# Optimization experiments

Hardware: AMD Instinct MI355X
Metric: run time of the kernel (lower is better)

Reference implementation:

```python
import jax, jax.numpy as jnp
import numpy as np


def _ln(x, g, b, eps=1e-5):
    mu = jnp.mean(x, axis=-1, keepdims=True)
    var = jnp.mean((x - mu) ** 2, axis=-1, keepdims=True)
    return (x - mu) * jax.lax.rsqrt(var + eps) * g + b


def setup_inputs() -> dict:
    key = jax.random.key(0)
    ks = jax.random.split(key, 12)
    B, H, W, D = 16, 128, 128, 64
    N = H * W
    Dff = 4 * D
    s = 0.02
    f32 = jnp.float32
    return {
        "x": jax.random.normal(ks[0], (B, N, D), f32),
        "H": H,
        "W": W,
        "ln1_scale": jnp.ones((D,), f32),
        "ln1_bias": jnp.zeros((D,), f32),
        "Wk": jax.random.normal(ks[1], (D, D), f32) * s,
        "bk": jnp.zeros((D,), f32),
        "Wq": jax.random.normal(ks[2], (D, D), f32) * s,
        "bq": jnp.zeros((D,), f32),
        "Wv": jax.random.normal(ks[3], (D, D), f32) * s,
        "bv": jnp.zeros((D,), f32),
        "Wr": jax.random.normal(ks[4], (D, D), f32) * s,
        "br": jnp.zeros((D,), f32),
        "ln2_scale": jnp.ones((D,), f32),
        "ln2_bias": jnp.zeros((D,), f32),
        "W1": jax.random.normal(ks[5], (Dff, D), f32) * s,
        "b1": jnp.zeros((Dff,), f32),
        "dw_w": jax.random.normal(ks[6], (Dff, 1, 3, 3), f32) * s,
        "dw_b": jnp.zeros((Dff,), f32),
        "W2": jax.random.normal(ks[7], (D, Dff), f32) * s,
        "b2": jnp.zeros((D,), f32),
    }


def reference(x, H, W, ln1_scale, ln1_bias, Wk, bk, Wq, bq, Wv, bv, Wr, br,
              ln2_scale, ln2_bias, W1, b1, dw_w, dw_b, W2, b2):
    B, N, D = x.shape
    Dff = W1.shape[0]

    # ---- EfficientAttention (head_count=1), tokens kept as [B, N, C] ----
    n1 = _ln(x, ln1_scale, ln1_bias)
    # 1x1 convs on [B,D,H,W] == per-token linear projections
    k = jax.nn.softmax(n1 @ Wk.T + bk, axis=1)    # softmax over spatial dim N (torch dim=2 of [B,Ck,N])
    q = jax.nn.softmax(n1 @ Wq.T + bq, axis=-1)   # softmax over key channels (torch dim=1)
    v = n1 @ Wv.T + bv                            # [B,N,Cv]
    context = jnp.einsum('bnk,bnv->bkv', k, v)    # key @ value^T, tiny [B,Ck,Cv]
    att = jnp.einsum('bkv,bnk->bnv', context, q)  # context^T @ query -> [B,N,Cv]
    attn_out = att @ Wr.T + br                    # reprojection 1x1 conv
    tx = x + attn_out

    # ---- MixFFN: fc1 -> depthwise 3x3 -> GELU -> fc2 ----
    n2 = _ln(tx, ln2_scale, ln2_bias)
    h = n2 @ W1.T + b1                            # [B,N,Dff]
    himg = jnp.transpose(h, (0, 2, 1)).reshape(B, Dff, H, W)
    conv = jax.lax.conv_general_dilated(
        himg, dw_w, window_strides=(1, 1), padding='SAME',
        feature_group_count=Dff,
        dimension_numbers=('NCHW', 'OIHW', 'NCHW')) + dw_b[None, :, None, None]
    h2 = jnp.transpose(conv.reshape(B, Dff, N), (0, 2, 1))
    h2 = jax.nn.gelu(h2, approximate=False)       # torch nn.GELU default is exact erf
    out = tx + (h2 @ W2.T + b2)
    return out
```

## Files before the change

### kernel.cpp

```cpp
#include <hip/hip_runtime.h>
#include <math.h>

typedef __bf16 bf16x8 __attribute__((ext_vector_type(8)));
typedef float f32x4 __attribute__((ext_vector_type(4)));
typedef float f32x2 __attribute__((ext_vector_type(2)));
typedef unsigned short u16x8 __attribute__((ext_vector_type(8)));
typedef unsigned short u16x4v __attribute__((ext_vector_type(4)));

constexpr int NIMG = 16384;
constexpr int HPITCH = 130;

__device__ __forceinline__ unsigned short f2bf(float f){
  unsigned u = __builtin_bit_cast(unsigned, f);
  u += 0x7fffu + ((u>>16)&1u);
  return (unsigned short)(u>>16);
}
__device__ __forceinline__ unsigned pack2(float a, float b){
  return (unsigned)f2bf(a) | ((unsigned)f2bf(b)<<16);
}
__device__ __forceinline__ float bf2f(unsigned short h){
  unsigned u = ((unsigned)h)<<16;
  return __builtin_bit_cast(float, u);
}
__device__ __forceinline__ bf16x8 ldfrag_g(const unsigned short* p){
  u16x8 v = *reinterpret_cast<const u16x8*>(p);
  return __builtin_bit_cast(bf16x8, v);
}
__device__ __forceinline__ f32x4 mfma16(bf16x8 a, bf16x8 b, f32x4 c){
  return __builtin_amdgcn_mfma_f32_16x16x32_bf16(a, b, c, 0, 0, 0);
}


__global__ __launch_bounds__(64) void k0_wfrag(
  const float* __restrict__ Wk, const float* __restrict__ Wq,
  const float* __restrict__ Wv, const float* __restrict__ Wr,
  const float* __restrict__ W1, const float* __restrict__ W2,
  const float* __restrict__ dww, const float* __restrict__ dwb,
  float* __restrict__ dwp, unsigned short* __restrict__ wf)
{
  const int bid = blockIdx.x, l = threadIdx.x;
  if (bid == 96){
    #pragma unroll
    for (int c=0;c<4;++c){
      int cp = l*4 + c;
      int f = ((cp&15)<<4) | (cp>>4);
      #pragma unroll
      for (int j=0;j<9;++j) dwp[cp*12 + j] = dww[f*9+j];
      dwp[cp*12 + 9]  = dwb[f];
      dwp[cp*12 + 10] = 0.f;
      dwp[cp*12 + 11] = 0.f;
    }
    return;
  }
  const float* src; int K, nt, ks; unsigned short* dst; bool perm = false;
  if (bid < 32){
    int w = bid>>3, f = bid&7;
    src = (w==0)?Wk:(w==1)?Wq:(w==2)?Wv:Wr;
    K = 64; nt = f>>1; ks = f&1;
    dst = wf + w*4096 + f*512;
  } else if (bid < 64){
    int f = bid-32; src = W1; K = 64; nt = f>>1; ks = f&1;
    dst = wf + 16384 + f*512;
  } else {
    int f = bid-64; src = W2; K = 256; nt = f>>3; ks = f&7;
    dst = wf + 32768 + f*512; perm = true;
  }
  u16x8 v;
  #pragma unroll
  for (int j=0;j<8;++j){
    int k = ks*32 + (l>>4)*8 + j;
    if (perm) k = ((k&15)<<4) | (k>>4);
    int n = nt*16 + (l&15);
    v[j] = f2bf(src[n*K + k]);
  }
  *reinterpret_cast<u16x8*>(dst + l*8) = v;
}

__global__ __launch_bounds__(256) void zhalo(unsigned* __restrict__ gh, unsigned* __restrict__ zr){
  int idx = blockIdx.x*256 + threadIdx.x;
  if (idx < 262144){
    int ch = idx & 63;
    int pos = idx >> 6;
    int side = pos & 1, row = pos >> 1;
    gh[(size_t)(row*HPITCH + side*(HPITCH-1))*64 + ch] = 0;
  } else {
    int j = idx - 262144;
    if (j < 8320) zr[j] = 0;
  }
}

__global__ __launch_bounds__(256,2) void k1_ctx(
  const float* __restrict__ x, const float* __restrict__ g1, const float* __restrict__ be1,
  const float* __restrict__ bk, const float* __restrict__ bv,
  const unsigned short* __restrict__ wf,
  float* __restrict__ g_part, float* __restrict__ g_sump)
{
  __shared__ unsigned short tiles[4][4096];
  __shared__ float ctx_l[64*68];
  __shared__ float ssum_l[4][64];
  const int t = threadIdx.x, wid = t>>6, l = t&63;
  const int lg = l>>4, l15 = l&15;
  unsigned short* tile = tiles[wid];
  const int tok0 = blockIdx.x*512 + wid*128;

  bf16x8 WkF[8], WvF[8];
  #pragma unroll
  for (int f=0; f<8; ++f){
    WkF[f] = ldfrag_g(wf +    0 + f*512 + l*8);
    WvF[f] = ldfrag_g(wf + 8192 + f*512 + l*8);
  }
  float4 g1v  = *reinterpret_cast<const float4*>(&g1[l15*4]);
  float4 be1v = *reinterpret_cast<const float4*>(&be1[l15*4]);
  float bkv[4], bvv[4];
  #pragma unroll
  for (int ct=0; ct<4; ++ct){ bkv[ct]=bk[ct*16+l15]; bvv[ct]=bv[ct*16+l15]; }

  f32x4 acc[4][4];
  #pragma unroll
  for (int a=0;a<4;++a)
    #pragma unroll
    for (int b=0;b<4;++b) acc[a][b] = (f32x4){0.f,0.f,0.f,0.f};
  float sume[4] = {0.f,0.f,0.f,0.f};

  for (int tb=0; tb<2; ++tb){
    const int tbase = tok0 + tb*64;
    #pragma unroll
    for (int it=0; it<16; ++it){
      int row = it*4 + lg;
      float4 xv = *reinterpret_cast<const float4*>(&x[(size_t)(tbase+row)*64 + l15*4]);
      float s1 = xv.x+xv.y+xv.z+xv.w;
      float s2 = xv.x*xv.x + xv.y*xv.y + xv.z*xv.z + xv.w*xv.w;
      #pragma unroll
      for (int off=1; off<16; off<<=1){ s1 += __shfl_xor(s1,off,64); s2 += __shfl_xor(s2,off,64); }
      float mu = s1*(1.f/64.f);
      float rs = rsqrtf(s2*(1.f/64.f) - mu*mu + 1e-5f);
      uint2 pk = { pack2((xv.x-mu)*rs*g1v.x + be1v.x, (xv.y-mu)*rs*g1v.y + be1v.y),
                   pack2((xv.z-mu)*rs*g1v.z + be1v.z, (xv.w-mu)*rs*g1v.w + be1v.w) };
      *reinterpret_cast<uint2*>(&tile[row*64 + ((l15*4) ^ ((row&7)<<3))]) = pk;
    }
    bf16x8 aF[4][2];
    #pragma unroll
    for (int mt=0;mt<4;++mt){
      int row = mt*16+l15, sw=(row&7)<<3, ab=row*64;
      aF[mt][0] = __builtin_bit_cast(bf16x8, *reinterpret_cast<const u16x8*>(tile+ab+((     lg*8)^sw)));
      aF[mt][1] = __builtin_bit_cast(bf16x8, *reinterpret_cast<const u16x8*>(tile+ab+((32 + lg*8)^sw)));
    }
    #pragma unroll
    for (int half=0; half<2; ++half){
      #pragma unroll
      for (int m2=0;m2<2;++m2){
        const int mt = half*2+m2;
        #pragma unroll
        for (int ct=0;ct<4;++ct){
          f32x4 z = {0.f,0.f,0.f,0.f};
          z = mfma16(aF[mt][0], WkF[ct*2+0], z);
          z = mfma16(aF[mt][1], WkF[ct*2+1], z);
          float e0=__expf(z[0]+bkv[ct]), e1=__expf(z[1]+bkv[ct]);
          float e2=__expf(z[2]+bkv[ct]), e3=__expf(z[3]+bkv[ct]);
          sume[ct] += (e0+e1)+(e2+e3);
          const int c = ct*16+l15, sw = (c&7)<<3;
          const int cb = m2*16+lg*4;
          uint2 pe = { pack2(e0,e1), pack2(e2,e3) };
          *reinterpret_cast<uint2*>(&tile[c*64 + (cb ^ sw)]) = pe;
          f32x4 w = {0.f,0.f,0.f,0.f};
          w = mfma16(aF[mt][0], WvF[ct*2+0], w);
          w = mfma16(aF[mt][1], WvF[ct*2+1], w);
          uint2 pv = { pack2(w[0]+bvv[ct], w[1]+bvv[ct]), pack2(w[2]+bvv[ct], w[3]+bvv[ct]) };
          *reinterpret_cast<uint2*>(&tile[c*64 + ((32+cb) ^ sw)]) = pv;
        }
      }
      bf16x8 eA[4], vB[4];
      #pragma unroll
      for (int cm=0;cm<4;++cm){
        int row = cm*16+l15, sw=(row&7)<<3;
        eA[cm] = __builtin_bit_cast(bf16x8, *reinterpret_cast<const u16x8*>(tile + row*64 + ((     lg*8)^sw)));
        vB[cm] = __builtin_bit_cast(bf16x8, *reinterpret_cast<const u16x8*>(tile + row*64 + ((32 + lg*8)^sw)));
      }
      #pragma unroll
      for (int cm=0; cm<4; ++cm)
        #pragma unroll
        for (int jn=0; jn<4; ++jn)
          acc[cm][jn] = mfma16(eA[cm], vB[jn], acc[cm][jn]);
    }
  }
  #pragma unroll
  for (int ct=0; ct<4; ++ct){
    float s = sume[ct];
    s += __shfl_xor(s,16,64); s += __shfl_xor(s,32,64);
    if (lg==0) ssum_l[wid][ct*16+l15] = s;
  }
  #define CTX_RED(OP) \
    _Pragma("unroll") for (int cm=0;cm<4;++cm) \
    _Pragma("unroll") for (int jn=0;jn<4;++jn) \
    _Pragma("unroll") for (int r=0;r<4;++r) \
      ctx_l[(cm*16+lg*4+r)*68 + jn*16+l15] OP acc[cm][jn][r];
  if (wid==0){ CTX_RED(=) }  __syncthreads();
  if (wid==1){ CTX_RED(+=) } __syncthreads();
  if (wid==2){ CTX_RED(+=) } __syncthreads();
  if (wid==3){ CTX_RED(+=) } __syncthreads();
  #undef CTX_RED
  for (int i=t; i<4096; i+=256)
    g_part[(size_t)blockIdx.x*4096 + i] = ctx_l[(i>>6)*68 + (i&63)];
  if (t<64)
    g_sump[blockIdx.x*64 + t] = ssum_l[0][t]+ssum_l[1][t]+ssum_l[2][t]+ssum_l[3][t];
}

__global__ __launch_bounds__(512) void k15_ctxwr(
  const float* __restrict__ g_part, const float* __restrict__ g_sump,
  const float* __restrict__ Wr, unsigned short* __restrict__ ctxWrF)
{
  __shared__ float sctx[4096];
  __shared__ float sWr[4096];
  __shared__ float sinv[64];
  const int b = blockIdx.x, t = threadIdx.x;
  if (t<64){
    float s=0.f;
    #pragma unroll 8
    for (int p=0;p<32;++p) s += g_sump[(b*32+p)*64 + t];
    sinv[t] = 1.f/s;
  }
  for (int idx=t; idx<4096; idx+=512){
    float s=0.f;
    #pragma unroll 8
    for (int p=0;p<32;++p) s += g_part[(size_t)(b*32+p)*4096 + idx];
    sctx[idx] = s;
  }
  __syncthreads();
  {
    int c = t>>3, d0 = (t&7)*8;
    float invc = sinv[c];
    #pragma unroll
    for (int dd=0; dd<8; ++dd){
      int d = d0+dd; float s = 0.f;
      #pragma unroll
      for (int v=0; v<64; ++v) s += sctx[c*64+v]*Wr[d*64+v];
      sWr[c*64+d] = s*invc;
    }
  }
  __syncthreads();
  {
    int f = t>>6, l = t&63, nt = f>>1, ks = f&1;
    u16x8 v;
    #pragma unroll
    for (int j=0;j<8;++j){
      int k = ks*32 + (l>>4)*8 + j;
      int n = nt*16 + (l&15);
      v[j] = f2bf(sWr[k*64+n]);
    }
    *reinterpret_cast<u16x8*>(ctxWrF + b*4096 + f*512 + l*8) = v;
  }
}

__global__ __launch_bounds__(256,2) void k2_attn_ffn1(
  const float* __restrict__ x,
  const float* __restrict__ g1, const float* __restrict__ be1,
  const float* __restrict__ bq, const float* __restrict__ br,
  const float* __restrict__ g2, const float* __restrict__ be2,
  const float* __restrict__ b1,
  const unsigned short* __restrict__ wf,
  const unsigned short* __restrict__ ctxWrF,
  unsigned short* __restrict__ g_txb, unsigned char* __restrict__ g_h)
{
  __shared__ unsigned short tiles[4][4096];
  const int t = threadIdx.x, wid = t>>6, l = t&63;
  const int l15 = l&15, lg = l>>4;
  unsigned short* tile = tiles[wid];
  const int tok0 = (blockIdx.x*4 + wid)*64;
  const int img  = blockIdx.x>>6;
  const int yrow = (tok0>>7)&127;
  const int xb   = tok0&127;
  const size_t hbase = ((size_t)(img*128 + yrow)*HPITCH + 1 + xb)*256;

  bf16x8 WqF[8], CWF[8];
  #pragma unroll
  for (int f=0; f<8; ++f){
    WqF[f] = ldfrag_g(wf + 4096 + f*512 + l*8);
    CWF[f] = ldfrag_g(ctxWrF + img*4096 + f*512 + l*8);
  }
  float4 g1v  = *reinterpret_cast<const float4*>(&g1[l15*4]);
  float4 be1v = *reinterpret_cast<const float4*>(&be1[l15*4]);
  float bqv[4], brv[4], g2v[4], be2v[4];
  #pragma unroll
  for (int nt=0; nt<4; ++nt){
    bqv[nt]=bq[nt*16+l15]; brv[nt]=br[nt*16+l15];
    g2v[nt]=g2[nt*16+l15]; be2v[nt]=be2[nt*16+l15];
  }
  float b1v[16];
  #pragma unroll
  for (int i=0;i<16;++i) b1v[i]=b1[i*16+l15];

  #pragma unroll
  for (int it=0; it<16; ++it){
    int row = it*4 + lg;
    float4 xv = *reinterpret_cast<const float4*>(&x[(size_t)(tok0+row)*64 + l15*4]);
    float s1 = xv.x+xv.y+xv.z+xv.w;
    float s2 = xv.x*xv.x + xv.y*xv.y + xv.z*xv.z + xv.w*xv.w;
    #pragma unroll
    for (int off=1; off<16; off<<=1){ s1 += __shfl_xor(s1,off,64); s2 += __shfl_xor(s2,off,64); }
    float mu = s1*(1.f/64.f);
    float rs = rsqrtf(s2*(1.f/64.f) - mu*mu + 1e-5f);
    uint2 pk = { pack2((xv.x-mu)*rs*g1v.x + be1v.x, (xv.y-mu)*rs*g1v.y + be1v.y),
                 pack2((xv.z-mu)*rs*g1v.z + be1v.z, (xv.w-mu)*rs*g1v.w + be1v.w) };
    *reinterpret_cast<uint2*>(&tile[row*64 + ((l15*4) ^ ((row&7)<<3))]) = pk;
  }

  for (int mt=0; mt<4; ++mt){
    const int arow = mt*16 + l15;
    const int asw  = (arow&7)<<3;
    const int abase= arow*64;
    bf16x8 a0 = __builtin_bit_cast(bf16x8, *reinterpret_cast<const u16x8*>(tile + abase + ((     lg*8) ^ asw)));
    bf16x8 a1 = __builtin_bit_cast(bf16x8, *reinterpret_cast<const u16x8*>(tile + abase + ((32 + lg*8) ^ asw)));
    f32x4 qa[4];
    #pragma unroll
    for (int nt=0; nt<4; ++nt){
      f32x4 z = {0.f,0.f,0.f,0.f};
      z = mfma16(a0, WqF[nt*2+0], z);
      z = mfma16(a1, WqF[nt*2+1], z);
      qa[nt] = z;
    }
    #pragma unroll
    for (int nt=0; nt<4; ++nt)
      #pragma unroll
      for (int r=0; r<4; ++r) qa[nt][r] += bqv[nt];
    float mx[4];
    #pragma unroll
    for (int r=0;r<4;++r) mx[r] = fmaxf(fmaxf(qa[0][r],qa[1][r]), fmaxf(qa[2][r],qa[3][r]));
    #pragma unroll
    for (int off=1; off<16; off<<=1)
      #pragma unroll
      for (int r=0;r<4;++r) mx[r] = fmaxf(mx[r], __shfl_xor(mx[r], off, 64));
    float sm[4] = {0.f,0.f,0.f,0.f};
    #pragma unroll
    for (int nt=0;nt<4;++nt)
      #pragma unroll
      for (int r=0;r<4;++r){ float e = __expf(qa[nt][r]-mx[r]); qa[nt][r]=e; sm[r]+=e; }
    #pragma unroll
    for (int off=1; off<16; off<<=1)
      #pragma unroll
      for (int r=0;r<4;++r) sm[r] += __shfl_xor(sm[r], off, 64);
    float inv[4];
    #pragma unroll
    for (int r=0;r<4;++r) inv[r] = 1.f/sm[r];
    #pragma unroll
    for (int nt=0;nt<4;++nt)
      #pragma unroll
      for (int r=0;r<4;++r){
        int row = mt*16 + lg*4 + r, col = nt*16 + l15;
        tile[row*64 + (col ^ ((row&7)<<3))] = f2bf(qa[nt][r]*inv[r]);
      }
    bf16x8 p0 = __builtin_bit_cast(bf16x8, *reinterpret_cast<const u16x8*>(tile + abase + ((     lg*8) ^ asw)));
    bf16x8 p1 = __builtin_bit_cast(bf16x8, *reinterpret_cast<const u16x8*>(tile + abase + ((32 + lg*8) ^ asw)));
    f32x4 ao[4];
    #pragma unroll
    for (int nt=0; nt<4; ++nt){
      f32x4 z = {0.f,0.f,0.f,0.f};
      z = mfma16(p0, CWF[nt*2+0], z);
      z = mfma16(p1, CWF[nt*2+1], z);
      ao[nt] = z;
    }
    float txv[4][4];
    float s1v[4] = {0.f,0.f,0.f,0.f}, s2v[4] = {0.f,0.f,0.f,0.f};
    #pragma unroll
    for (int nt=0;nt<4;++nt)
      #pragma unroll
      for (int r=0;r<4;++r){
        size_t row = (size_t)(tok0 + mt*16 + lg*4 + r);
        float v = ao[nt][r] + brv[nt] + x[row*64 + nt*16+l15];
        g_txb[row*64 + nt*16+l15] = f2bf(v);
        txv[nt][r] = v; s1v[r] += v; s2v[r] += v*v;
      }
    #pragma unroll
    for (int off=1; off<16; off<<=1)
      #pragma unroll
      for (int r=0;r<4;++r){ s1v[r] += __shfl_xor(s1v[r], off, 64); s2v[r] += __shfl_xor(s2v[r], off, 64); }
    #pragma unroll
    for (int r=0;r<4;++r){
      float mu2 = s1v[r]*(1.f/64.f);
      float rs  = rsqrtf(s2v[r]*(1.f/64.f) - mu2*mu2 + 1e-5f);
      s1v[r] = mu2; s2v[r] = rs;
    }
    #pragma unroll
    for (int nt=0;nt<4;++nt)
      #pragma unroll
      for (int r=0;r<4;++r){
        int row = mt*16 + lg*4 + r, col = nt*16 + l15;
        float n2 = (txv[nt][r]-s1v[r])*s2v[r]*g2v[nt] + be2v[nt];
        tile[row*64 + (col ^ ((row&7)<<3))] = f2bf(n2);
      }
  }

  for (int mt=0; mt<4; ++mt){
    const int arow = mt*16 + l15;
    const int asw  = (arow&7)<<3;
    const int abase= arow*64;
    bf16x8 n20 = __builtin_bit_cast(bf16x8, *reinterpret_cast<const u16x8*>(tile + abase + ((     lg*8) ^ asw)));
    bf16x8 n21 = __builtin_bit_cast(bf16x8, *reinterpret_cast<const u16x8*>(tile + abase + ((32 + lg*8) ^ asw)));
    unsigned hq[4][4];
    #pragma unroll
    for (int np=0; np<8; ++np){
      bf16x8 wa0 = ldfrag_g(wf + 16384 + (np*4+0)*512 + l*8);
      bf16x8 wa1 = ldfrag_g(wf + 16384 + (np*4+1)*512 + l*8);
      bf16x8 wb0 = ldfrag_g(wf + 16384 + (np*4+2)*512 + l*8);
      bf16x8 wb1 = ldfrag_g(wf + 16384 + (np*4+3)*512 + l*8);
      float ba = b1v[np*2], bb = b1v[np*2+1];
      f32x4 ha = {ba,ba,ba,ba};
      ha = mfma16(n20, wa0, ha);
      ha = mfma16(n21, wa1, ha);
      f32x4 hb = {bb,bb,bb,bb};
      hb = mfma16(n20, wb0, hb);
      hb = mfma16(n21, wb1, hb);
      const int d = np>>1;
      if ((np&1)==0){
        #pragma unroll
        for (int r=0;r<4;++r)
          hq[r][d] = (unsigned)__builtin_amdgcn_cvt_pk_fp8_f32(ha[r], hb[r], 0, false);
      } else {
        #pragma unroll
        for (int r=0;r<4;++r)
          hq[r][d] = (unsigned)__builtin_amdgcn_cvt_pk_fp8_f32(ha[r], hb[r], (int)hq[r][d], true);
      }
    }
    #pragma unroll
    for (int r=0;r<4;++r){
      const size_t ro = hbase + (size_t)(mt*16+lg*4+r)*256 + l15*16;
      uint4 v = { hq[r][0], hq[r][1], hq[r][2], hq[r][3] };
      *reinterpret_cast<uint4*>(g_h + ro) = v;
    }
  }
}

__global__ __launch_bounds__(256,3) void k3_conv_ffn2(
  const unsigned char* __restrict__ g_h,
  const unsigned char* __restrict__ zrow,
  const float* __restrict__ dwp,
  const float* __restrict__ b2,
  const unsigned short* __restrict__ wf,
  const unsigned short* __restrict__ g_txb, float* __restrict__ out)
{
  __shared__ unsigned ring[4][2322];
  __shared__ unsigned short obuf[2][4096];
  const int t = threadIdx.x, w = t>>6, l = t&63;
  const int l15 = l&15, lg = l>>4;
  const int bid = (blockIdx.x & 7)*128 + (blockIdx.x >> 3);
  const int img = bid>>6;
  const int r6  = bid&63;
  const int y0  = (r6>>3)*16, x0 = (r6&7)*16;

  const float4 tA = *reinterpret_cast<const float4*>(&dwp[t*12]);
  const float4 tB = *reinterpret_cast<const float4*>(&dwp[t*12+4]);
  const float4 tC = *reinterpret_cast<const float4*>(&dwp[t*12+8]);

  bf16x8 W2F[8];
  #pragma unroll
  for (int q=0;q<8;++q)
    W2F[q] = ldfrag_g(wf + 32768 + (w*8 + q)*512 + l*8);
  const float4 b2q = *reinterpret_cast<const float4*>(&b2[w*16 + lg*4]);

  const int pi = 1 + (t&15);
  const int c0 = (t>>4)*16;

  auto rowsrc = [&](int ri) -> const unsigned char* {
    return (ri>=0 && ri<128)
      ? g_h + ((size_t)(img*128+ri)*HPITCH + x0)*256
      : zrow + x0*256;
  };
  auto ldrow = [&](int ri, uint4* m, unsigned* h){
    const unsigned char* src = rowsrc(ri);
    *m = *reinterpret_cast<const uint4*>(src + pi*256 + c0);
    if (t < 128){
      int ph = (t<64)?0:17, dh = t&63;
      *h = reinterpret_cast<const unsigned*>(src + ph*256)[dh];
    }
  };
  auto cvtwr = [&](unsigned* rg, int base, unsigned mdw){
    f32x2 lo = __builtin_amdgcn_cvt_pk_f32_fp8((int)mdw, false);
    f32x2 hi = __builtin_amdgcn_cvt_pk_f32_fp8((int)mdw, true);
    unsigned plo, phi;
    asm("v_cvt_pk_bf16_f32 %0, %1, %2" : "=v"(plo) : "v"(lo[0]), "v"(lo[1]));
    asm("v_cvt_pk_bf16_f32 %0, %1, %2" : "=v"(phi) : "v"(hi[0]), "v"(hi[1]));
    rg[base]   = plo;
    rg[base+1] = phi;
  };
  auto wrrow = [&](int sl, uint4 m, unsigned h){
    unsigned* rg = ring[sl];
    const int base = pi*129 + (c0>>1);
    #pragma unroll
    for (int d=0; d<4; ++d) cvtwr(rg, base + 2*d, m[d]);
    if (t < 128){
      int ph = (t<64)?0:17, dh = t&63;
      cvtwr(rg, ph*129 + 2*dh, h);
    }
  };

  {
    uint4 m0,m1,m2; unsigned h0=0,h1=0,h2=0;
    ldrow(y0-1,&m0,&h0); ldrow(y0,&m1,&h1); ldrow(y0+1,&m2,&h2);
    wrrow(0,m0,h0); wrrow(1,m1,h1); wrrow(2,m2,h2);
  }
  __syncthreads();

  for (int yy=0; yy<16; ++yy){
    const int gy = y0 + yy;
    uint4 rm; unsigned rh = 0;
    ldrow(gy+2, &rm, &rh);
    const size_t gtok = (size_t)img*16384 + (size_t)gy*128 + x0 + l15;
    const u16x4v tq = *reinterpret_cast<const u16x4v*>(&g_txb[gtok*64 + w*16 + lg*4]);

    const unsigned short* rA16 = reinterpret_cast<const unsigned short*>(ring[(yy  )&3]);
    const unsigned short* rB16 = reinterpret_cast<const unsigned short*>(ring[(yy+1)&3]);
    const unsigned short* rC16 = reinterpret_cast<const unsigned short*>(ring[(yy+2)&3]);
    unsigned short* ob = obuf[yy&1];

    float pA=bf2f(rA16[t]),     pB=bf2f(rB16[t]),     pC=bf2f(rC16[t]);
    float cA=bf2f(rA16[258+t]), cB=bf2f(rB16[258+t]), cC=bf2f(rC16[258+t]);
    unsigned short qA=rA16[516+t], qB=rB16[516+t], qC=rC16[516+t];
    #pragma unroll
    for (int s=0;s<16;++s){
      const int o = (s<15 ? (s+3) : 17)*258 + t;
      unsigned short zA=rA16[o], zB=rB16[o], zC=rC16[o];
      float nA=bf2f(qA), nB=bf2f(qB), nC=bf2f(qC);
      float a = tC.y;
      a = fmaf(tA.x,pA, a); a = fmaf(tA.y,cA, a); a = fmaf(tA.z,nA, a);
      a = fmaf(tA.w,pB, a); a = fmaf(tB.x,cB, a); a = fmaf(tB.y,nB, a);
      a = fmaf(tB.z,pC, a); a = fmaf(tB.w,cC, a); a = fmaf(tC.x,nC, a);
      float u2 = a*a;
      float arg = a*(-2.3022082f - 0.1029432f*u2);
      float e = __builtin_amdgcn_exp2f(arg);
      float g = a*__builtin_amdgcn_rcpf(1.f + e);
      ob[s*256 + (t ^ ((s&7)<<3))] = f2bf(g);
      pA=cA; pB=cB; pC=cC; cA=nA; cB=nB; cC=nC; qA=zA; qB=zB; qC=zC;
    }

    wrrow((yy+3)&3, rm, rh);
    __syncthreads();

    f32x4 oacc = {0.f,0.f,0.f,0.f};
    const int nsw = (l15&7)<<3;
    #pragma unroll
    for (int i=0;i<4;++i){
      bf16x8 fb0 = __builtin_bit_cast(bf16x8,
        *reinterpret_cast<const u16x8*>(&ob[l15*256 + ((i*64      + lg*8) ^ nsw)]));
      bf16x8 fb1 = __builtin_bit_cast(bf16x8,
        *reinterpret_cast<const u16x8*>(&ob[l15*256 + ((i*64 + 32 + lg*8) ^ nsw)]));
      oacc = mfma16(W2F[i*2+0], fb0, oacc);
      oacc = mfma16(W2F[i*2+1], fb1, oacc);
    }
    float4 o;
    o.x = oacc[0] + b2q.x + bf2f(tq[0]);
    o.y = oacc[1] + b2q.y + bf2f(tq[1]);
    o.z = oacc[2] + b2q.z + bf2f(tq[2]);
    o.w = oacc[3] + b2q.w + bf2f(tq[3]);
    *reinterpret_cast<float4*>(&out[gtok*64 + w*16 + lg*4]) = o;
  }
}

extern "C" void kernel_launch(void* const* d_in, const int* in_sizes, int n_in,
                              void* d_out, int out_size, void* d_ws, size_t ws_size,
                              hipStream_t stream)
{
  const float* x  =(const float*)d_in[0];
  const float* g1 =(const float*)d_in[3];
  const float* be1=(const float*)d_in[4];
  const float* Wk =(const float*)d_in[5];
  const float* bk =(const float*)d_in[6];
  const float* Wq =(const float*)d_in[7];
  const float* bq =(const float*)d_in[8];
  const float* Wv =(const float*)d_in[9];
  const float* bv =(const float*)d_in[10];
  const float* Wr =(const float*)d_in[11];
  const float* br =(const float*)d_in[12];
  const float* g2 =(const float*)d_in[13];
  const float* be2=(const float*)d_in[14];
  const float* W1 =(const float*)d_in[15];
  const float* b1 =(const float*)d_in[16];
  const float* dww=(const float*)d_in[17];
  const float* dwb=(const float*)d_in[18];
  const float* W2 =(const float*)d_in[19];
  const float* b2 =(const float*)d_in[20];
  float* outp = (float*)d_out;
  char* ws = (char*)d_ws;

  unsigned short* wfb    = (unsigned short*)ws;
  unsigned short* ctxWrF = (unsigned short*)(ws + 98304);
  float* g_sump = (float*)(ws + 229376);
  float* g_part = (float*)(ws + 393216);
  unsigned short* g_txb = (unsigned short*)(ws + 16777216);
  unsigned char* g_h    = (unsigned char*)(ws + 50331648);
  unsigned char* zr     = (unsigned char*)(ws + 186646528);
  float* dwp            = (float*)(ws + 186712064);

  hipLaunchKernelGGL(k0_wfrag, dim3(97), dim3(64), 0, stream, Wk, Wq, Wv, Wr, W1, W2, dww, dwb, dwp, wfb);
  hipLaunchKernelGGL(zhalo, dim3(1057), dim3(256), 0, stream, (unsigned*)g_h, (unsigned*)zr);
  hipLaunchKernelGGL(k1_ctx, dim3(512), dim3(256), 0, stream, x, g1, be1, bk, bv, wfb, g_part, g_sump);
  hipLaunchKernelGGL(k15_ctxwr, dim3(16), dim3(512), 0, stream, g_part, g_sump, Wr, ctxWrF);
  hipLaunchKernelGGL(k2_attn_ffn1, dim3(1024), dim3(256), 0, stream,
                     x, g1, be1, bq, br, g2, be2, b1, wfb, ctxWrF, g_txb, g_h);
  hipLaunchKernelGGL(k3_conv_ffn2, dim3(1024), dim3(256), 0, stream,
                     g_h, zr, dwp, b2, wfb, g_txb, outp);
}
```

Before: 209.9 us.

## Keep FP8 in LDS ring and compute depthwise conv on channel pairs

The LDS ring buffer now holds raw FP8 bytes instead of converting them to BF16 at write time, which halves the ring size. The depthwise 3x3 conv is reworked so each thread handles two channels across 8 pixels, using packed f32x2 math and packed BF16 stores. Conv weights are re-laid out in interleaved pairs to match. The smaller shared-memory footprint allows the launch bound to rise to 4 blocks per CU, at the cost of FP8 decode work inside the inner loop and possible LDS bank conflicts on 16-bit reads.

Measured after the change: 208.3 us. About the same (-0.8%).

```diff
diff --git a/kernel.cpp b/kernel.cpp
--- a/kernel.cpp
+++ b/kernel.cpp
@@ -41,14 +41,18 @@
   const int bid = blockIdx.x, l = threadIdx.x;
   if (bid == 96){
     #pragma unroll
-    for (int c=0;c<4;++c){
-      int cp = l*4 + c;
-      int f = ((cp&15)<<4) | (cp>>4);
-      #pragma unroll
-      for (int j=0;j<9;++j) dwp[cp*12 + j] = dww[f*9+j];
-      dwp[cp*12 + 9]  = dwb[f];
-      dwp[cp*12 + 10] = 0.f;
-      dwp[cp*12 + 11] = 0.f;
+    for (int h=0; h<2; ++h){
+      int cp = l + h*64;
+      #pragma unroll
+      for (int b=0; b<2; ++b){
+        int slot = 2*cp + b;
+        int f = ((slot&15)<<4) | (slot>>4);
+        #pragma unroll
+        for (int j=0;j<9;++j) dwp[cp*24 + j*2 + b] = dww[f*9+j];
+        dwp[cp*24 + 18 + b] = dwb[f];
+        dwp[cp*24 + 20 + b] = 0.f;
+        dwp[cp*24 + 22 + b] = 0.f;
+      }
     }
     return;
   }
@@ -429,7 +433,7 @@
   }
 }
 
-__global__ __launch_bounds__(256,3) void k3_conv_ffn2(
+__global__ __launch_bounds__(256,4) void k3_conv_ffn2(
   const unsigned char* __restrict__ g_h,
   const unsigned char* __restrict__ zrow,
   const float* __restrict__ dwp,
@@ -437,7 +441,7 @@
   const unsigned short* __restrict__ wf,
   const unsigned short* __restrict__ g_txb, float* __restrict__ out)
 {
-  __shared__ unsigned ring[4][2322];
+  __shared__ unsigned ring[4][1170];
   __shared__ unsigned short obuf[2][4096];
   const int t = threadIdx.x, w = t>>6, l = t&63;
   const int l15 = l&15, lg = l>>4;
@@ -446,9 +450,13 @@
   const int r6  = bid&63;
   const int y0  = (r6>>3)*16, x0 = (r6&7)*16;
 
-  const float4 tA = *reinterpret_cast<const float4*>(&dwp[t*12]);
-  const float4 tB = *reinterpret_cast<const float4*>(&dwp[t*12+4]);
-  const float4 tC = *reinterpret_cast<const float4*>(&dwp[t*12+8]);
+  const int cp = t & 127;
+  const int pg = t >> 7;
+  f32x2 tp[9];
+  #pragma unroll
+  for (int j=0;j<9;++j)
+    tp[j] = *reinterpret_cast<const f32x2*>(&dwp[cp*24 + j*2]);
+  const f32x2 cb2 = *reinterpret_cast<const f32x2*>(&dwp[cp*24 + 18]);
 
   bf16x8 W2F[8];
   #pragma unroll
@@ -472,23 +480,13 @@
       *h = reinterpret_cast<const unsigned*>(src + ph*256)[dh];
     }
   };
-  auto cvtwr = [&](unsigned* rg, int base, unsigned mdw){
-    f32x2 lo = __builtin_amdgcn_cvt_pk_f32_fp8((int)mdw, false);
-    f32x2 hi = __builtin_amdgcn_cvt_pk_f32_fp8((int)mdw, true);
-    unsigned plo, phi;
-    asm("v_cvt_pk_bf16_f32 %0, %1, %2" : "=v"(plo) : "v"(lo[0]), "v"(lo[1]));
-    asm("v_cvt_pk_bf16_f32 %0, %1, %2" : "=v"(phi) : "v"(hi[0]), "v"(hi[1]));
-    rg[base]   = plo;
-    rg[base+1] = phi;
-  };
   auto wrrow = [&](int sl, uint4 m, unsigned h){
     unsigned* rg = ring[sl];
-    const int base = pi*129 + (c0>>1);
-    #pragma unroll
-    for (int d=0; d<4; ++d) cvtwr(rg, base + 2*d, m[d]);
+    const int base = pi*65 + (c0>>2);
+    rg[base+0] = m.x; rg[base+1] = m.y; rg[base+2] = m.z; rg[base+3] = m.w;
     if (t < 128){
       int ph = (t<64)?0:17, dh = t&63;
-      cvtwr(rg, ph*129 + 2*dh, h);
+      rg[ph*65 + dh] = h;
     }
   };
 
@@ -498,6 +496,9 @@
     wrrow(0,m0,h0); wrrow(1,m1,h1); wrrow(2,m2,h2);
   }
   __syncthreads();
+
+  const f32x2 kC0 = {-2.3022082f,-2.3022082f};
+  const f32x2 kC1 = {-0.1029432f,-0.1029432f};
 
   for (int yy=0; yy<16; ++yy){
     const int gy = y0 + yy;
@@ -506,29 +507,43 @@
     const size_t gtok = (size_t)img*16384 + (size_t)gy*128 + x0 + l15;
     const u16x4v tq = *reinterpret_cast<const u16x4v*>(&g_txb[gtok*64 + w*16 + lg*4]);
 
-    const unsigned short* rA16 = reinterpret_cast<const unsigned short*>(ring[(yy  )&3]);
-    const unsigned short* rB16 = reinterpret_cast<const unsigned short*>(ring[(yy+1)&3]);
-    const unsigned short* rC16 = reinterpret_cast<const unsigned short*>(ring[(yy+2)&3]);
-    unsigned short* ob = obuf[yy&1];
-
-    float pA=bf2f(rA16[t]),     pB=bf2f(rB16[t]),     pC=bf2f(rC16[t]);
-    float cA=bf2f(rA16[258+t]), cB=bf2f(rB16[258+t]), cC=bf2f(rC16[258+t]);
-    unsigned short qA=rA16[516+t], qB=rB16[516+t], qC=rC16[516+t];
-    #pragma unroll
-    for (int s=0;s<16;++s){
-      const int o = (s<15 ? (s+3) : 17)*258 + t;
-      unsigned short zA=rA16[o], zB=rB16[o], zC=rC16[o];
-      float nA=bf2f(qA), nB=bf2f(qB), nC=bf2f(qC);
-      float a = tC.y;
-      a = fmaf(tA.x,pA, a); a = fmaf(tA.y,cA, a); a = fmaf(tA.z,nA, a);
-      a = fmaf(tA.w,pB, a); a = fmaf(tB.x,cB, a); a = fmaf(tB.y,nB, a);
-      a = fmaf(tB.z,pC, a); a = fmaf(tB.w,cC, a); a = fmaf(tC.x,nC, a);
-      float u2 = a*a;
-      float arg = a*(-2.3022082f - 0.1029432f*u2);
-      float e = __builtin_amdgcn_exp2f(arg);
-      float g = a*__builtin_amdgcn_rcpf(1.f + e);
-      ob[s*256 + (t ^ ((s&7)<<3))] = f2bf(g);
-      pA=cA; pB=cB; pC=cC; cA=nA; cB=nB; cC=nC; qA=zA; qB=zB; qC=zC;
+    {
+      const unsigned short* rA = reinterpret_cast<const unsigned short*>(ring[(yy  )&3]);
+      const unsigned short* rB = reinterpret_cast<const unsigned short*>(ring[(yy+1)&3]);
+      const unsigned short* rC = reinterpret_cast<const unsigned short*>(ring[(yy+2)&3]);
+      unsigned short* ob = obuf[yy&1];
+      const int rb = pg*8;
+      f32x2 PA = __builtin_amdgcn_cvt_pk_f32_fp8((int)rA[(rb  )*130 + cp], false);
+      f32x2 PB = __builtin_amdgcn_cvt_pk_f32_fp8((int)rB[(rb  )*130 + cp], false);
+      f32x2 PC = __builtin_amdgcn_cvt_pk_f32_fp8((int)rC[(rb  )*130 + cp], false);
+      f32x2 CA = __builtin_amdgcn_cvt_pk_f32_fp8((int)rA[(rb+1)*130 + cp], false);
+      f32x2 CB = __builtin_amdgcn_cvt_pk_f32_fp8((int)rB[(rb+1)*130 + cp], false);
+      f32x2 CC = __builtin_amdgcn_cvt_pk_f32_fp8((int)rC[(rb+1)*130 + cp], false);
+      #pragma unroll
+      for (int i=0;i<8;++i){
+        const int ro = (rb+i+2)*130 + cp;
+        f32x2 NA = __builtin_amdgcn_cvt_pk_f32_fp8((int)rA[ro], false);
+        f32x2 NB = __builtin_amdgcn_cvt_pk_f32_fp8((int)rB[ro], false);
+        f32x2 NC = __builtin_amdgcn_cvt_pk_f32_fp8((int)rC[ro], false);
+        f32x2 a = cb2;
+        a += tp[0]*PA; a += tp[1]*CA; a += tp[2]*NA;
+        a += tp[3]*PB; a += tp[4]*CB; a += tp[5]*NB;
+        a += tp[6]*PC; a += tp[7]*CC; a += tp[8]*NC;
+        f32x2 u = a*a;
+        f32x2 wv = u*kC1 + kC0;
+        f32x2 arg = a*wv;
+        f32x2 e;
+        e[0]=__builtin_amdgcn_exp2f(arg[0]); e[1]=__builtin_amdgcn_exp2f(arg[1]);
+        f32x2 den = e + (f32x2){1.f,1.f};
+        f32x2 rc;
+        rc[0]=__builtin_amdgcn_rcpf(den[0]); rc[1]=__builtin_amdgcn_rcpf(den[1]);
+        f32x2 g = a*rc;
+        unsigned pk;
+        asm("v_cvt_pk_bf16_f32 %0, %1, %2" : "=v"(pk) : "v"(g[0]), "v"(g[1]));
+        const int p = rb + i;
+        *reinterpret_cast<unsigned*>(&ob[p*256 + ((2*cp) ^ ((p&7)<<3))]) = pk;
+        PA=CA; PB=CB; PC=CC; CA=NA; CB=NB; CC=NC;
+      }
     }
 
     wrrow((yy+3)&3, rm, rh);
@@ -536,6 +551,7 @@
 
     f32x4 oacc = {0.f,0.f,0.f,0.f};
     const int nsw = (l15&7)<<3;
+    const unsigned short* ob = obuf[yy&1];
     #pragma unroll
     for (int i=0;i<4;++i){
       bf16x8 fb0 = __builtin_bit_cast(bf16x8,
```
